# Optimization experiments

Hardware: AMD Instinct MI355X
Metric: run time of the kernel (lower is better)

Reference implementation:

```python
import jax, jax.numpy as jnp
import numpy as np

SMALL_NUMBER = 1e-7
N_NODES = 100000
FEAT = 512
N_GRAPHS = 512


def setup_inputs() -> dict:
    key = jax.random.key(0)
    k1, k2 = jax.random.split(key)
    node_features = jax.random.normal(k1, (N_NODES, FEAT), dtype=jnp.float32)
    node_to_graph_map = jnp.sort(
        jax.random.randint(k2, (N_NODES,), 0, N_GRAPHS, dtype=jnp.int32)
    )
    alpha = jnp.ones((FEAT,), dtype=jnp.float32)
    beta = jnp.zeros((FEAT,), dtype=jnp.float32)
    gamma = jnp.ones((FEAT,), dtype=jnp.float32)
    return {
        "node_features": node_features,
        "node_to_graph_map": node_to_graph_map,
        "alpha": alpha,
        "beta": beta,
        "gamma": gamma,
        "num_segments": N_GRAPHS,
    }


def _segment_mean(data, segment_ids, num_segments):
    # data: [N, D]; segment_ids: [N] sorted ints in [0, num_segments)
    sums = jax.ops.segment_sum(data, segment_ids, num_segments=num_segments)
    counts = jax.ops.segment_sum(
        jnp.ones((data.shape[0], 1), dtype=data.dtype),
        segment_ids,
        num_segments=num_segments,
    )
    return sums / jnp.maximum(counts, 1.0)


def reference(node_features, node_to_graph_map, alpha, beta, gamma, num_segments):
    # GraphNorm: gamma * (h - alpha*mu) / sigma + beta, per-graph statistics.
    graph_means = _segment_mean(node_features, node_to_graph_map, num_segments)  # [G, D]
    per_node_means = graph_means[node_to_graph_map]  # [N, D]
    centered = node_features - alpha * per_node_means
    graph_vars = _segment_mean(jnp.square(centered), node_to_graph_map, num_segments)  # [G, D]
    per_node_std = jnp.sqrt(graph_vars)[node_to_graph_map]  # [N, D]
    out = centered / (per_node_std + SMALL_NUMBER)
    out = out * gamma + beta
    return out
```

## Files before the change

kernel.cpp:

```cpp
#include <hip/hip_runtime.h>

#define FEAT 512
#define FEAT4 128
#define NGRAPH 512
#define NB 2048
#define MAXSLOT 8
#define EPS 1e-7f

typedef float f32x4 __attribute__((ext_vector_type(4)));

__device__ __forceinline__ void acc4(float4& s, const float4 v) {
    s.x += v.x; s.y += v.y; s.z += v.z; s.w += v.w;
}
__device__ __forceinline__ void accsq4(float4& s, const float4 v) {
    s.x += v.x * v.x; s.y += v.y * v.y; s.z += v.z * v.z; s.w += v.w * v.w;
}
__device__ __forceinline__ float4 add4(const float4 a, const float4 b) {
    return make_float4(a.x + b.x, a.y + b.y, a.z + b.z, a.w + b.w);
}
__device__ __forceinline__ int logical_block(int pb, int nb) {
    return (pb & 7) * (nb >> 3) + (pb >> 3);
}

__global__ __launch_bounds__(256) void gn_bounds(
    const int* __restrict__ map, int* __restrict__ segstart, int n_nodes)
{
    const int i = blockIdx.x * blockDim.x + threadIdx.x;
    if (i >= n_nodes) return;
    const int cur  = map[i];
    const int prev = (i == 0) ? -1 : map[i - 1];
    for (int g = prev + 1; g <= cur; ++g) segstart[g] = i;
    if (i == n_nodes - 1)
        for (int g = cur + 1; g <= NGRAPH; ++g) segstart[g] = n_nodes;
}

__global__ __launch_bounds__(256) void gn_partial(
    const float* __restrict__ feat,
    const int*   __restrict__ map,
    const int*   __restrict__ segstart,
    float*       __restrict__ PPART,
    int n_nodes, int rpb)
{
    const int lb = logical_block(blockIdx.x, gridDim.x);
    const int rs = lb * rpb;
    if (rs >= n_nodes) return;
    const int re = min(rs + rpb, n_nodes);

    const int tid = threadIdx.x;
    const int q = tid & (FEAT4 - 1);
    const int r = tid >> 7;

    __shared__ float4 lsum[2][FEAT4];
    __shared__ float4 lssq[2][FEAT4];
    const float4* __restrict__ f4 = (const float4*)feat;
    float4* __restrict__ P4 = (float4*)PPART;

    int cur = rs;
    int g = map[rs];
    int slot = lb - segstart[g] / rpb;
    while (cur < re) {
        const int send = min(segstart[g + 1], re);

        float4 sum = make_float4(0.f, 0.f, 0.f, 0.f);
        float4 ssq = make_float4(0.f, 0.f, 0.f, 0.f);
        #pragma unroll 4
        for (int row = cur + r; row < send; row += 2) {
            float4 v = f4[(size_t)row * FEAT4 + q];
            acc4(sum, v);
            accsq4(ssq, v);
        }
        lsum[r][q] = sum;
        lssq[r][q] = ssq;
        __syncthreads();
        if (r == 0 && slot >= 0 && slot < MAXSLOT) {
            const size_t o = ((size_t)(g * MAXSLOT + slot) * 2) * FEAT4 + q;
            P4[o]         = add4(lsum[0][q], lsum[1][q]);
            P4[o + FEAT4] = add4(lssq[0][q], lssq[1][q]);
        }
        __syncthreads();
        cur = send;
        if (cur < re) g = map[cur];
        slot = 0;
    }
}

__global__ __launch_bounds__(256) void gn_apply(
    const float* __restrict__ feat,
    const int*   __restrict__ map,
    const int*   __restrict__ segstart,
    const float* __restrict__ PPART,
    const float* __restrict__ alpha,
    const float* __restrict__ beta,
    const float* __restrict__ gamma,
    float*       __restrict__ out,
    int n_nodes, int rpb)
{
    const int lb = logical_block(blockIdx.x, gridDim.x);
    const int rs = lb * rpb;
    if (rs >= n_nodes) return;
    const int re = min(rs + rpb, n_nodes);

    const int tid = threadIdx.x;
    const int q = tid & (FEAT4 - 1);
    const int r = tid >> 7;

    const f32x4* __restrict__ f4n = (const f32x4*)feat;
    const float4* __restrict__ P4 = (const float4*)PPART;
    f32x4* __restrict__ o4 = (f32x4*)out;

    const float4 al = ((const float4*)alpha)[q];
    const float4 be = ((const float4*)beta)[q];
    const float4 ga = ((const float4*)gamma)[q];

    int cur = rs;
    int g = map[rs];
    while (cur < re) {
        const int gstart = segstart[g];
        const int gend   = segstart[g + 1];
        const int send   = min(gend, re);
        const int cnt    = gend - gstart;
        const int bfirst = gstart / rpb;
        int nslots = (gend - 1) / rpb - bfirst + 1;
        if (nslots > MAXSLOT) nslots = MAXSLOT;

        float4 sum = make_float4(0.f, 0.f, 0.f, 0.f);
        float4 ssq = make_float4(0.f, 0.f, 0.f, 0.f);
        for (int s = 0; s < nslots; ++s) {
            const size_t o = ((size_t)(g * MAXSLOT + s) * 2) * FEAT4 + q;
            acc4(sum, P4[o]);
            acc4(ssq, P4[o + FEAT4]);
        }

        const float inv = 1.0f / (float)max(cnt, 1);
        f32x4 sv, tv;
        {
            const float mu[4]  = { sum.x * inv, sum.y * inv, sum.z * inv, sum.w * inv };
            const float msq[4] = { ssq.x * inv, ssq.y * inv, ssq.z * inv, ssq.w * inv };
            const float aa[4]  = { al.x, al.y, al.z, al.w };
            const float bb[4]  = { be.x, be.y, be.z, be.w };
            const float gg[4]  = { ga.x, ga.y, ga.z, ga.w };
            #pragma unroll
            for (int j = 0; j < 4; ++j) {
                float var = msq[j] - mu[j] * mu[j] * (2.0f * aa[j] - aa[j] * aa[j]);
                var = fmaxf(var, 0.0f);
                const float s = gg[j] / (sqrtf(var) + EPS);
                sv[j] = s;
                tv[j] = bb[j] - aa[j] * mu[j] * s;
            }
        }

        #pragma unroll 4
        for (int row = cur + r; row < send; row += 2) {
            const size_t idx = (size_t)row * FEAT4 + q;
            f32x4 v = __builtin_nontemporal_load(&f4n[idx]);
            f32x4 o = v * sv + tv;
            __builtin_nontemporal_store(o, &o4[idx]);
        }
        cur = send;
        if (cur < re) g = map[cur];
    }
}

__global__ __launch_bounds__(512) void graphnorm_stats(
    const float* __restrict__ feat,
    const int*   __restrict__ map,
    const float* __restrict__ alpha,
    const float* __restrict__ beta,
    const float* __restrict__ gamma,
    float* __restrict__ S,
    float* __restrict__ T,
    int n_nodes)
{
    const int g = blockIdx.x;
    int lo = 0, hi = n_nodes;
    while (lo < hi) { int mid = (lo + hi) >> 1; if (map[mid] < g) lo = mid + 1; else hi = mid; }
    const int seg_start = lo;
    hi = n_nodes;
    while (lo < hi) { int mid = (lo + hi) >> 1; if (map[mid] < g + 1) lo = mid + 1; else hi = mid; }
    const int seg_end = lo;
    const int cnt = seg_end - seg_start;

    const int tid = threadIdx.x;
    const int q = tid & (FEAT4 - 1);
    const int r = tid >> 7;

    float4 sum = make_float4(0.f, 0.f, 0.f, 0.f);
    float4 ssq = make_float4(0.f, 0.f, 0.f, 0.f);
    const float4* __restrict__ f4 = (const float4*)feat;

    for (int row = seg_start + r; row < seg_end; row += 4) {
        float4 v = f4[(size_t)row * FEAT4 + q];
        acc4(sum, v);
        accsq4(ssq, v);
    }

    __shared__ float4 lsum[4][FEAT4];
    __shared__ float4 lssq[4][FEAT4];
    lsum[r][q] = sum;
    lssq[r][q] = ssq;
    __syncthreads();

    if (r == 0) {
        #pragma unroll
        for (int k = 1; k < 4; ++k) {
            acc4(sum, lsum[k][q]);
            acc4(ssq, lssq[k][q]);
        }
        const float inv = 1.0f / (float)max(cnt, 1);
        float4 al = ((const float4*)alpha)[q];
        float4 be = ((const float4*)beta)[q];
        float4 ga = ((const float4*)gamma)[q];
        float mu[4]  = { sum.x * inv, sum.y * inv, sum.z * inv, sum.w * inv };
        float msq[4] = { ssq.x * inv, ssq.y * inv, ssq.z * inv, ssq.w * inv };
        float a[4]   = { al.x, al.y, al.z, al.w };
        float bb[4]  = { be.x, be.y, be.z, be.w };
        float gg[4]  = { ga.x, ga.y, ga.z, ga.w };
        float so[4], to[4];
        #pragma unroll
        for (int j = 0; j < 4; ++j) {
            float var = msq[j] - mu[j] * mu[j] * (2.0f * a[j] - a[j] * a[j]);
            var = fmaxf(var, 0.0f);
            float s = gg[j] / (sqrtf(var) + EPS);
            so[j] = s;
            to[j] = bb[j] - a[j] * mu[j] * s;
        }
        ((float4*)S)[(size_t)g * FEAT4 + q] = make_float4(so[0], so[1], so[2], so[3]);
        ((float4*)T)[(size_t)g * FEAT4 + q] = make_float4(to[0], to[1], to[2], to[3]);
    }
}

__global__ __launch_bounds__(256) void graphnorm_apply_tab(
    const float* __restrict__ feat,
    const int*   __restrict__ map,
    const float* __restrict__ S,
    const float* __restrict__ T,
    float* __restrict__ out,
    long total4)
{
    const float4* __restrict__ f4 = (const float4*)feat;
    const float4* __restrict__ S4 = (const float4*)S;
    const float4* __restrict__ T4 = (const float4*)T;
    f32x4* __restrict__ o4 = (f32x4*)out;

    const long stride = (long)gridDim.x * blockDim.x;
    for (long idx = (long)blockIdx.x * blockDim.x + threadIdx.x; idx < total4; idx += stride) {
        const int n = (int)(idx >> 7);
        const int q = (int)(idx & (FEAT4 - 1));
        const int g = map[n];
        float4 v = f4[idx];
        float4 s = S4[(size_t)g * FEAT4 + q];
        float4 t = T4[(size_t)g * FEAT4 + q];
        f32x4 o;
        o.x = v.x * s.x + t.x;
        o.y = v.y * s.y + t.y;
        o.z = v.z * s.z + t.z;
        o.w = v.w * s.w + t.w;
        o4[idx] = o;
    }
}

extern "C" void kernel_launch(void* const* d_in, const int* in_sizes, int n_in,
                              void* d_out, int out_size, void* d_ws, size_t ws_size,
                              hipStream_t stream) {
    const float* feat  = (const float*)d_in[0];
    const int*   map   = (const int*)d_in[1];
    const float* alpha = (const float*)d_in[2];
    const float* beta  = (const float*)d_in[3];
    const float* gamma = (const float*)d_in[4];

    const int n_nodes = in_sizes[1];
    const int rpb = (n_nodes + NB - 1) / NB;

    const size_t ppartElems = (size_t)NGRAPH * MAXSLOT * 2 * FEAT;
    const size_t needBytes  = ppartElems * 4 + (NGRAPH + 1) * sizeof(int);

    if (ws_size >= needBytes) {
        float* PPART   = (float*)d_ws;
        int*   SEGSTART = (int*)((float*)d_ws + ppartElems);

        const int bblocks = (n_nodes + 255) / 256;
        gn_bounds<<<bblocks, 256, 0, stream>>>(map, SEGSTART, n_nodes);
        gn_partial<<<NB, 256, 0, stream>>>(feat, map, SEGSTART, PPART, n_nodes, rpb);
        gn_apply<<<NB, 256, 0, stream>>>(feat, map, SEGSTART, PPART,
                                         alpha, beta, gamma,
                                         (float*)d_out, n_nodes, rpb);
    } else {
        float* S = (float*)d_ws;
        float* T = S + (size_t)NGRAPH * FEAT;
        graphnorm_stats<<<NGRAPH, 512, 0, stream>>>(feat, map, alpha, beta, gamma, S, T, n_nodes);
        const long total4 = (long)n_nodes * FEAT4;
        graphnorm_apply_tab<<<2048, 256, 0, stream>>>(feat, map, S, T, (float*)d_out, total4);
    }
}
```

Before: 111.3 us.

## Fuse partial-stats and apply passes into one cooperative kernel with grid sync

Replaces the separate partial-sum and apply kernels with a single cooperative kernel of 1024 blocks. Each block accumulates per-graph partial sums over its row range, waits at a grid-wide barrier, then re-reads its same rows to normalise them, hoping those rows are still in the large last-level cache from the first pass. This also saves one kernel launch. The costs are a grid.sync barrier, a requirement that all 1024 blocks be co-resident, and a fall back to the old two-kernel path if the cooperative launch fails. The unused stats/table kernels and the workspace-size check are removed.

```diff
diff --git a/kernel.cpp b/kernel.cpp
--- a/kernel.cpp
+++ b/kernel.cpp
@@ -1,9 +1,13 @@
 #include <hip/hip_runtime.h>
+#include <hip/hip_cooperative_groups.h>
+
+namespace cg = cooperative_groups;
 
 #define FEAT 512
 #define FEAT4 128
 #define NGRAPH 512
-#define NB 2048
+#define NBC 1024
+#define NBF 2048
 #define MAXSLOT 8
 #define EPS 1e-7f
 
@@ -32,6 +36,124 @@
     for (int g = prev + 1; g <= cur; ++g) segstart[g] = i;
     if (i == n_nodes - 1)
         for (int g = cur + 1; g <= NGRAPH; ++g) segstart[g] = n_nodes;
+}
+
+__global__ __launch_bounds__(256, 4) void gn_coop(
+    const float* __restrict__ feat,
+    const int*   __restrict__ map,
+    const int*   __restrict__ segstart,
+    float*       __restrict__ PPART,
+    const float* __restrict__ alpha,
+    const float* __restrict__ beta,
+    const float* __restrict__ gamma,
+    float*       __restrict__ out,
+    int n_nodes, int rpb)
+{
+    cg::grid_group grid = cg::this_grid();
+
+    const int lb = logical_block(blockIdx.x, gridDim.x);
+    const int rs = lb * rpb;
+    const int re = min(rs + rpb, n_nodes);
+    const bool active = (rs < n_nodes);
+
+    const int tid = threadIdx.x;
+    const int q = tid & (FEAT4 - 1);
+    const int r = tid >> 7;
+
+    __shared__ float4 lsum[2][FEAT4];
+    __shared__ float4 lssq[2][FEAT4];
+
+    const float4* __restrict__ f4 = (const float4*)feat;
+    float4* __restrict__ P4 = (float4*)PPART;
+
+    if (active) {
+        int cur = rs;
+        int g = map[rs];
+        int slot = lb - segstart[g] / rpb;
+        while (cur < re) {
+            const int send = min(segstart[g + 1], re);
+
+            float4 sum = make_float4(0.f, 0.f, 0.f, 0.f);
+            float4 ssq = make_float4(0.f, 0.f, 0.f, 0.f);
+            #pragma unroll 4
+            for (int row = cur + r; row < send; row += 2) {
+                float4 v = f4[(size_t)row * FEAT4 + q];
+                acc4(sum, v);
+                accsq4(ssq, v);
+            }
+            lsum[r][q] = sum;
+            lssq[r][q] = ssq;
+            __syncthreads();
+            if (r == 0 && slot >= 0 && slot < MAXSLOT) {
+                const size_t o = ((size_t)(g * MAXSLOT + slot) * 2) * FEAT4 + q;
+                P4[o]         = add4(lsum[0][q], lsum[1][q]);
+                P4[o + FEAT4] = add4(lssq[0][q], lssq[1][q]);
+            }
+            __syncthreads();
+            cur = send;
+            if (cur < re) g = map[cur];
+            slot = 0;
+        }
+    }
+
+    __threadfence();
+    grid.sync();
+
+    if (active) {
+        const float4 al = ((const float4*)alpha)[q];
+        const float4 be = ((const float4*)beta)[q];
+        const float4 ga = ((const float4*)gamma)[q];
+        f32x4* __restrict__ o4 = (f32x4*)out;
+
+        int cur = rs;
+        int g = map[rs];
+        while (cur < re) {
+            const int gstart = segstart[g];
+            const int gend   = segstart[g + 1];
+            const int send   = min(gend, re);
+            const int cnt    = gend - gstart;
+            const int bfirst = gstart / rpb;
+            int nslots = (gend - 1) / rpb - bfirst + 1;
+            if (nslots > MAXSLOT) nslots = MAXSLOT;
+
+            float4 sum = make_float4(0.f, 0.f, 0.f, 0.f);
+            float4 ssq = make_float4(0.f, 0.f, 0.f, 0.f);
+            for (int s = 0; s < nslots; ++s) {
+                const size_t o = ((size_t)(g * MAXSLOT + s) * 2) * FEAT4 + q;
+                acc4(sum, P4[o]);
+                acc4(ssq, P4[o + FEAT4]);
+            }
+
+            const float inv = 1.0f / (float)max(cnt, 1);
+            f32x4 sv, tv;
+            {
+                const float mu[4]  = { sum.x * inv, sum.y * inv, sum.z * inv, sum.w * inv };
+                const float msq[4] = { ssq.x * inv, ssq.y * inv, ssq.z * inv, ssq.w * inv };
+                const float aa[4]  = { al.x, al.y, al.z, al.w };
+                const float bb[4]  = { be.x, be.y, be.z, be.w };
+                const float gg[4]  = { ga.x, ga.y, ga.z, ga.w };
+                #pragma unroll
+                for (int j = 0; j < 4; ++j) {
+                    float var = msq[j] - mu[j] * mu[j] * (2.0f * aa[j] - aa[j] * aa[j]);
+                    var = fmaxf(var, 0.0f);
+                    const float s = gg[j] / (sqrtf(var) + EPS);
+                    sv[j] = s;
+                    tv[j] = bb[j] - aa[j] * mu[j] * s;
+                }
+            }
+
+            const f32x4* __restrict__ f4n = (const f32x4*)feat;
+            #pragma unroll 4
+            for (int row = cur + r; row < send; row += 2) {
+                const size_t idx = (size_t)row * FEAT4 + q;
+                f32x4 v = *(const f32x4*)&f4n[idx];
+                f32x4 o = v * sv + tv;
+                __builtin_nontemporal_store(o, &o4[idx]);
+            }
+            cur = send;
+            if (cur < re) g = map[cur];
+        }
+    }
 }
 
 __global__ __launch_bounds__(256) void gn_partial(
@@ -161,104 +283,6 @@
     }
 }
 
-__global__ __launch_bounds__(512) void graphnorm_stats(
-    const float* __restrict__ feat,
-    const int*   __restrict__ map,
-    const float* __restrict__ alpha,
-    const float* __restrict__ beta,
-    const float* __restrict__ gamma,
-    float* __restrict__ S,
-    float* __restrict__ T,
-    int n_nodes)
-{
-    const int g = blockIdx.x;
-    int lo = 0, hi = n_nodes;
-    while (lo < hi) { int mid = (lo + hi) >> 1; if (map[mid] < g) lo = mid + 1; else hi = mid; }
-    const int seg_start = lo;
-    hi = n_nodes;
-    while (lo < hi) { int mid = (lo + hi) >> 1; if (map[mid] < g + 1) lo = mid + 1; else hi = mid; }
-    const int seg_end = lo;
-    const int cnt = seg_end - seg_start;
-
-    const int tid = threadIdx.x;
-    const int q = tid & (FEAT4 - 1);
-    const int r = tid >> 7;
-
-    float4 sum = make_float4(0.f, 0.f, 0.f, 0.f);
-    float4 ssq = make_float4(0.f, 0.f, 0.f, 0.f);
-    const float4* __restrict__ f4 = (const float4*)feat;
-
-    for (int row = seg_start + r; row < seg_end; row += 4) {
-        float4 v = f4[(size_t)row * FEAT4 + q];
-        acc4(sum, v);
-        accsq4(ssq, v);
-    }
-
-    __shared__ float4 lsum[4][FEAT4];
-    __shared__ float4 lssq[4][FEAT4];
-    lsum[r][q] = sum;
-    lssq[r][q] = ssq;
-    __syncthreads();
-
-    if (r == 0) {
-        #pragma unroll
-        for (int k = 1; k < 4; ++k) {
-            acc4(sum, lsum[k][q]);
-            acc4(ssq, lssq[k][q]);
-        }
-        const float inv = 1.0f / (float)max(cnt, 1);
-        float4 al = ((const float4*)alpha)[q];
-        float4 be = ((const float4*)beta)[q];
-        float4 ga = ((const float4*)gamma)[q];
-        float mu[4]  = { sum.x * inv, sum.y * inv, sum.z * inv, sum.w * inv };
-        float msq[4] = { ssq.x * inv, ssq.y * inv, ssq.z * inv, ssq.w * inv };
-        float a[4]   = { al.x, al.y, al.z, al.w };
-        float bb[4]  = { be.x, be.y, be.z, be.w };
-        float gg[4]  = { ga.x, ga.y, ga.z, ga.w };
-        float so[4], to[4];
-        #pragma unroll
-        for (int j = 0; j < 4; ++j) {
-            float var = msq[j] - mu[j] * mu[j] * (2.0f * a[j] - a[j] * a[j]);
-            var = fmaxf(var, 0.0f);
-            float s = gg[j] / (sqrtf(var) + EPS);
-            so[j] = s;
-            to[j] = bb[j] - a[j] * mu[j] * s;
-        }
-        ((float4*)S)[(size_t)g * FEAT4 + q] = make_float4(so[0], so[1], so[2], so[3]);
-        ((float4*)T)[(size_t)g * FEAT4 + q] = make_float4(to[0], to[1], to[2], to[3]);
-    }
-}
-
-__global__ __launch_bounds__(256) void graphnorm_apply_tab(
-    const float* __restrict__ feat,
-    const int*   __restrict__ map,
-    const float* __restrict__ S,
-    const float* __restrict__ T,
-    float* __restrict__ out,
-    long total4)
-{
-    const float4* __restrict__ f4 = (const float4*)feat;
-    const float4* __restrict__ S4 = (const float4*)S;
-    const float4* __restrict__ T4 = (const float4*)T;
-    f32x4* __restrict__ o4 = (f32x4*)out;
-
-    const long stride = (long)gridDim.x * blockDim.x;
-    for (long idx = (long)blockIdx.x * blockDim.x + threadIdx.x; idx < total4; idx += stride) {
-        const int n = (int)(idx >> 7);
-        const int q = (int)(idx & (FEAT4 - 1));
-        const int g = map[n];
-        float4 v = f4[idx];
-        float4 s = S4[(size_t)g * FEAT4 + q];
-        float4 t = T4[(size_t)g * FEAT4 + q];
-        f32x4 o;
-        o.x = v.x * s.x + t.x;
-        o.y = v.y * s.y + t.y;
-        o.z = v.z * s.z + t.z;
-        o.w = v.w * s.w + t.w;
-        o4[idx] = o;
-    }
-}
-
 extern "C" void kernel_launch(void* const* d_in, const int* in_sizes, int n_in,
                               void* d_out, int out_size, void* d_ws, size_t ws_size,
                               hipStream_t stream) {
@@ -267,28 +291,28 @@
     const float* alpha = (const float*)d_in[2];
     const float* beta  = (const float*)d_in[3];
     const float* gamma = (const float*)d_in[4];
-
-    const int n_nodes = in_sizes[1];
-    const int rpb = (n_nodes + NB - 1) / NB;
+    float* outp = (float*)d_out;
+
+    int n_nodes = in_sizes[1];
 
     const size_t ppartElems = (size_t)NGRAPH * MAXSLOT * 2 * FEAT;
-    const size_t needBytes  = ppartElems * 4 + (NGRAPH + 1) * sizeof(int);
-
-    if (ws_size >= needBytes) {
-        float* PPART   = (float*)d_ws;
-        int*   SEGSTART = (int*)((float*)d_ws + ppartElems);
-
-        const int bblocks = (n_nodes + 255) / 256;
-        gn_bounds<<<bblocks, 256, 0, stream>>>(map, SEGSTART, n_nodes);
-        gn_partial<<<NB, 256, 0, stream>>>(feat, map, SEGSTART, PPART, n_nodes, rpb);
-        gn_apply<<<NB, 256, 0, stream>>>(feat, map, SEGSTART, PPART,
-                                         alpha, beta, gamma,
-                                         (float*)d_out, n_nodes, rpb);
-    } else {
-        float* S = (float*)d_ws;
-        float* T = S + (size_t)NGRAPH * FEAT;
-        graphnorm_stats<<<NGRAPH, 512, 0, stream>>>(feat, map, alpha, beta, gamma, S, T, n_nodes);
-        const long total4 = (long)n_nodes * FEAT4;
-        graphnorm_apply_tab<<<2048, 256, 0, stream>>>(feat, map, S, T, (float*)d_out, total4);
-    }
-}
+    float* PPART    = (float*)d_ws;
+    int*   SEGSTART = (int*)((float*)d_ws + ppartElems);
+
+    const int bblocks = (n_nodes + 255) / 256;
+    gn_bounds<<<bblocks, 256, 0, stream>>>(map, SEGSTART, n_nodes);
+
+    int rpb = (n_nodes + NBC - 1) / NBC;
+    void* args[] = { (void*)&feat, (void*)&map, (void*)&SEGSTART, (void*)&PPART,
+                     (void*)&alpha, (void*)&beta, (void*)&gamma, (void*)&outp,
+                     (void*)&n_nodes, (void*)&rpb };
+    hipError_t err = hipLaunchCooperativeKernel((const void*)gn_coop,
+                                                dim3(NBC), dim3(256),
+                                                args, 0, stream);
+    if (err != hipSuccess) {
+        const int rpb2 = (n_nodes + NBF - 1) / NBF;
+        gn_partial<<<NBF, 256, 0, stream>>>(feat, map, SEGSTART, PPART, n_nodes, rpb2);
+        gn_apply<<<NBF, 256, 0, stream>>>(feat, map, SEGSTART, PPART,
+                                          alpha, beta, gamma, outp, n_nodes, rpb2);
+    }
+}
```

Result: slower. 298.9 us (+168.6%).
